# Performance work log

Hardware: AMD Instinct MI355X
Metric: run time of the kernel (lower is better)

The kernel has to match this reference:

```python
import jax, jax.numpy as jnp
import numpy as np

B, H, S, D = 2, 8, 4096, 64

def setup_inputs() -> dict:
    key = jax.random.key(0)
    kq, kk, kv = jax.random.split(key, 3)
    queries = jax.random.normal(kq, (B, H, S, D), dtype=jnp.float32)
    keys = jax.random.normal(kk, (B, H, S, D), dtype=jnp.float32)
    values = jax.random.normal(kv, (B, H, S, D), dtype=jnp.float32)
    adj = jnp.zeros((1,), dtype=jnp.int32)  # unused by the module, kept for signature fidelity
    return {"queries": queries, "keys": keys, "values": values, "adj": adj}

def reference(queries, keys, values, adj):
    # scores: [B,H,S,S]; note the original divides by a hard-coded 16, not sqrt(d)
    scores = jnp.einsum('bhqd,bhkd->bhqk', queries, keys) / 16.0
    attn = jax.nn.softmax(scores, axis=-1)
    # dropout p=0.0 -> identity in eval/deterministic mode
    h = jnp.einsum('bhqk,bhkd->bhqd', attn, values)  # [B,H,S,D]
    # original uses .view (a reshape, NOT a transpose) to (S, B, H, D)
    return jnp.reshape(h, (S, B, H, D))
```

## Files before the change

kernel.cpp:

```cpp
#include <hip/hip_runtime.h>
#include <hip/hip_bf16.h>
#include <math.h>

#define S_LEN 4096
#define D_DIM 64
#define NBH   16
#define HKT   32
#define QPRE  0.09016844f

typedef __attribute__((ext_vector_type(8))) short bf16x8;
typedef __attribute__((ext_vector_type(4))) float f32x4;
typedef __attribute__((ext_vector_type(16))) float f32x16;
typedef __attribute__((ext_vector_type(8))) __fp16 f16x8;
typedef __attribute__((ext_vector_type(2))) __fp16 f16x2;
typedef __attribute__((ext_vector_type(2))) unsigned int u32x2;

__device__ __forceinline__ unsigned int pkbf(float lo, float hi) {
  unsigned int ua = __float_as_uint(lo) + 0x8000u;
  unsigned int ub = __float_as_uint(hi) + 0x8000u;
  return __builtin_amdgcn_perm(ub, ua, 0x07060302u);
}
__device__ __forceinline__ unsigned int pkhf(float lo, float hi) {
  f16x2 h = __builtin_amdgcn_cvt_pkrtz(lo, hi);
  return *(unsigned int*)&h;
}
__device__ __forceinline__ void dma16(const unsigned short* g, unsigned short* l) {
  __builtin_amdgcn_global_load_lds(
      (const __attribute__((address_space(1))) unsigned int*)g,
      (__attribute__((address_space(3))) unsigned int*)l, 16, 0, 0);
}

__global__ __launch_bounds__(256) void prep(const float* __restrict__ K,
                                            const float* __restrict__ V,
                                            unsigned short* __restrict__ Kbf,
                                            unsigned short* __restrict__ Vt) {
  const int tid = threadIdx.x;
  __shared__ unsigned short tile[64][72];
  if (blockIdx.x < 256) {
    const int bh = blockIdx.x >> 4, ch = blockIdx.x & 15;
    const size_t base = ((size_t)bh * S_LEN + ch * 256) * D_DIM;
#pragma unroll
    for (int p = 0; p < 8; ++p) {
      int i = tid + p * 256;
      int row = i >> 3, c = (i & 7) * 8;
      float4 a = *(const float4*)&K[base + row * D_DIM + c];
      float4 b = *(const float4*)&K[base + row * D_DIM + c + 4];
      uint4 w;
      w.x = pkbf(a.x, a.y); w.y = pkbf(a.z, a.w);
      w.z = pkbf(b.x, b.y); w.w = pkbf(b.z, b.w);
      *(uint4*)&Kbf[base + row * D_DIM + c] = w;
    }
    return;
  }
  const int blk = blockIdx.x - 256;
  const int bh = blk >> 6, kt = blk & 63;
  const float* src = V + ((size_t)bh * S_LEN + kt * 64) * D_DIM;
#pragma unroll
  for (int p = 0; p < 4; ++p) {
    int i = tid + p * 256;
    int row = i >> 4, c = (i & 15) * 4;
    float4 f = *(const float4*)&src[row * D_DIM + c];
    int cs = c ^ (((row >> 4) & 3) << 4);
    unsigned long long w = (unsigned long long)pkhf(f.x, f.y) |
                           ((unsigned long long)pkhf(f.z, f.w) << 32);
    *(unsigned long long*)&tile[row][cs] = w;
  }
  __syncthreads();
  const int kc = tid & 7;
#pragma unroll
  for (int p = 0; p < 2; ++p) {
    int d = p * 32 + (tid >> 3);
    int col = d ^ (((kc >> 1) & 3) << 4);
    union { unsigned short u[8]; uint4 v; } t;
#pragma unroll
    for (int i = 0; i < 8; ++i) t.u[i] = tile[kc * 8 + i][col];
    *(uint4*)&Vt[((size_t)bh * D_DIM + d) * S_LEN + kt * 64 + kc * 8] = t.v;
  }
}

__global__ __launch_bounds__(256, 4) void fattn(const float* __restrict__ Q,
                                                const unsigned short* __restrict__ Kbf,
                                                const unsigned short* __restrict__ Vt,
                                                unsigned short* __restrict__ Oh,
                                                float* __restrict__ Lw) {
  const int bh   = blockIdx.x & 15;
  const int qb   = (blockIdx.x >> 4) & 31;
  const int half = blockIdx.x >> 9;
  const int tid  = threadIdx.x;
  const int wave = tid >> 6;
  const int lane = tid & 63;
  const int l31  = lane & 31;
  const int hi   = lane >> 5;
  const int T0   = half * HKT;

  __shared__ unsigned short Ksh[2][64][64];
  __shared__ unsigned short Vsh[2][64][64];

  bf16x8 qf2[4];
  {
    const int qg = qb * 128 + wave * 32 + l31;
    const float* qp = Q + ((size_t)bh * S_LEN + qg) * D_DIM + hi * 8;
#pragma unroll
    for (int dm = 0; dm < 4; ++dm) {
      float4 a = *(const float4*)&qp[dm * 16];
      float4 b = *(const float4*)&qp[dm * 16 + 4];
      union { unsigned int u[4]; bf16x8 v; } f;
      f.u[0] = pkbf(a.x * QPRE, a.y * QPRE);
      f.u[1] = pkbf(a.z * QPRE, a.w * QPRE);
      f.u[2] = pkbf(b.x * QPRE, b.y * QPRE);
      f.u[3] = pkbf(b.z * QPRE, b.w * QPRE);
      qf2[dm] = f.v;
    }
  }

  f32x16 ov[2] = {{}, {}};
  float Lt = 0.f;

  const unsigned short* Kb = Kbf + (size_t)bh * S_LEN * D_DIM;
  const unsigned short* Vb = Vt + (size_t)bh * D_DIM * S_LEN;

  const int r_lo = wave * 8 + (lane >> 3);
  const int csrc = ((lane & 7) ^ (lane >> 3)) * 8;

#define DMAK(T, B) do { const int t_ = (T); \
  dma16(&Kb[(size_t)(t_ * 64 + r_lo) * 64 + csrc],      &Ksh[B][wave * 8][0]); \
  dma16(&Kb[(size_t)(t_ * 64 + r_lo + 32) * 64 + csrc], &Ksh[B][wave * 8 + 32][0]); } while (0)
#define DMAV(T, B) do { const int t_ = (T); \
  dma16(&Vb[(size_t)r_lo * S_LEN + t_ * 64 + csrc],        &Vsh[B][wave * 8][0]); \
  dma16(&Vb[(size_t)(r_lo + 32) * S_LEN + t_ * 64 + csrc], &Vsh[B][wave * 8 + 32][0]); } while (0)

#define SCORES(KB, PD) do { \
  const char* kbase_ = (const char*)&Ksh[KB][0][0]; \
  _Pragma("unroll") \
  for (int kt2 = 0; kt2 < 2; ++kt2) { \
    const int krow_ = kt2 * 32 + l31; \
    f32x16 acc2 = {}; \
    _Pragma("unroll") \
    for (int dm = 0; dm < 4; ++dm) { \
      bf16x8 kf = *(const bf16x8*)(kbase_ + krow_ * 128 + (((dm * 2 + hi) ^ (krow_ & 7)) * 16)); \
      acc2 = __builtin_amdgcn_mfma_f32_32x32x16_bf16(kf, qf2[dm], acc2, 0, 0, 0); \
    } \
    float pp[16]; \
    _Pragma("unroll") \
    for (int j = 0; j < 16; ++j) pp[j] = __builtin_amdgcn_exp2f(acc2[j]); \
    Lt += (((pp[0] + pp[1]) + (pp[2] + pp[3])) + ((pp[4] + pp[5]) + (pp[6] + pp[7]))) \
        + (((pp[8] + pp[9]) + (pp[10] + pp[11])) + ((pp[12] + pp[13]) + (pp[14] + pp[15]))); \
    unsigned int w00 = pkhf(pp[0], pp[1]),   w01 = pkhf(pp[2], pp[3]); \
    unsigned int w10 = pkhf(pp[4], pp[5]),   w11 = pkhf(pp[6], pp[7]); \
    unsigned int w20 = pkhf(pp[8], pp[9]),   w21 = pkhf(pp[10], pp[11]); \
    unsigned int w30 = pkhf(pp[12], pp[13]), w31 = pkhf(pp[14], pp[15]); \
    u32x2 s0 = __builtin_amdgcn_permlane32_swap(w00, w10, false, false); \
    u32x2 s1 = __builtin_amdgcn_permlane32_swap(w01, w11, false, false); \
    u32x2 s2 = __builtin_amdgcn_permlane32_swap(w20, w30, false, false); \
    u32x2 s3 = __builtin_amdgcn_permlane32_swap(w21, w31, false, false); \
    PD[kt2 * 2 + 0][0] = s0.x; PD[kt2 * 2 + 0][1] = s1.x; \
    PD[kt2 * 2 + 0][2] = s0.y; PD[kt2 * 2 + 0][3] = s1.y; \
    PD[kt2 * 2 + 1][0] = s2.x; PD[kt2 * 2 + 1][1] = s3.x; \
    PD[kt2 * 2 + 1][2] = s2.y; PD[kt2 * 2 + 1][3] = s3.y; \
  } } while (0)

#define PVSTEP(VB, PU) do { \
  const char* vbase_ = (const char*)&Vsh[VB][0][0]; \
  _Pragma("unroll") \
  for (int dt2 = 0; dt2 < 2; ++dt2) { \
    const int drow_ = dt2 * 32 + l31; \
    _Pragma("unroll") \
    for (int s4 = 0; s4 < 4; ++s4) { \
      f16x8 va = *(const f16x8*)(vbase_ + drow_ * 128 + (((s4 * 2 + hi) ^ (drow_ & 7)) * 16)); \
      union { unsigned int u[4]; f16x8 v; } pb; \
      pb.u[0] = PU[s4][0]; pb.u[1] = PU[s4][1]; \
      pb.u[2] = PU[s4][2]; pb.u[3] = PU[s4][3]; \
      ov[dt2] = __builtin_amdgcn_mfma_f32_32x32x16_f16(va, pb.v, ov[dt2], 0, 0, 0); \
    } \
  } } while (0)

  unsigned int pA[4][4];

  DMAK(T0, 0); DMAV(T0, 0);
  __syncthreads();

  for (int b = 0; b < HKT - 2; b += 2) {
    DMAK(T0 + b + 1, 1); DMAV(T0 + b + 1, 1);
    SCORES(0, pA);
    PVSTEP(0, pA);
    __syncthreads();
    DMAK(T0 + b + 2, 0); DMAV(T0 + b + 2, 0);
    SCORES(1, pA);
    PVSTEP(1, pA);
    __syncthreads();
  }
  DMAK(T0 + HKT - 1, 1); DMAV(T0 + HKT - 1, 1);
  SCORES(0, pA);
  PVSTEP(0, pA);
  __syncthreads();
  SCORES(1, pA);
  PVSTEP(1, pA);

  Lt += __shfl_xor(Lt, 32);
  const size_t grow = (size_t)bh * S_LEN + qb * 128 + wave * 32 + l31;
  if (lane < 32) Lw[grow * 2 + half] = Lt;
#pragma unroll
  for (int dt2 = 0; dt2 < 2; ++dt2)
#pragma unroll
    for (int m = 0; m < 4; ++m) {
      uint2 w;
      w.x = pkhf(ov[dt2][4 * m + 0], ov[dt2][4 * m + 1]);
      w.y = pkhf(ov[dt2][4 * m + 2], ov[dt2][4 * m + 3]);
      *(uint2*)&Oh[grow * 128 + half * 64 + dt2 * 32 + m * 8 + hi * 4] = w;
    }
#undef DMAK
#undef DMAV
#undef SCORES
#undef PVSTEP
}

__global__ __launch_bounds__(256) void reduce(unsigned short* Oh, const float* __restrict__ Lw) {
  const int tid = threadIdx.x;
  const size_t r = (size_t)blockIdx.x * 32 + (tid >> 3);
  const int d0 = (tid & 7) * 8;
  union { uint4 v; __fp16 h[8]; } a, b;
  a.v = *(const uint4*)&Oh[r * 128 + d0];
  b.v = *(const uint4*)&Oh[r * 128 + 64 + d0];
  const float linv = 1.0f / (Lw[r * 2] + Lw[r * 2 + 1]);
  float o[8];
#pragma unroll
  for (int j = 0; j < 8; ++j) o[j] = ((float)a.h[j] + (float)b.h[j]) * linv;
  __syncthreads();
  float* Of = (float*)Oh;
  float4 w0 = {o[0], o[1], o[2], o[3]};
  float4 w1 = {o[4], o[5], o[6], o[7]};
  *(float4*)&Of[r * 64 + d0]     = w0;
  *(float4*)&Of[r * 64 + d0 + 4] = w1;
}

extern "C" void kernel_launch(void* const* d_in, const int* in_sizes, int n_in,
                              void* d_out, int out_size, void* d_ws, size_t ws_size,
                              hipStream_t stream) {
  const float* Q = (const float*)d_in[0];
  const float* K = (const float*)d_in[1];
  const float* V = (const float*)d_in[2];
  unsigned short* Kbf = (unsigned short*)d_ws;
  unsigned short* Vt  = Kbf + (size_t)NBH * S_LEN * D_DIM;
  float* Lw = (float*)(Vt + (size_t)NBH * S_LEN * D_DIM);
  unsigned short* Oh = (unsigned short*)d_out;

  prep<<<1280, 256, 0, stream>>>(K, V, Kbf, Vt);
  fattn<<<NBH * 32 * 2, 256, 0, stream>>>(Q, Kbf, Vt, Oh, Lw);
  reduce<<<(NBH * S_LEN) / 32, 256, 0, stream>>>(Oh, Lw);
}
```

Baseline: 178.1 us.

## Process two query sub-tiles per wave to reuse K/V fragments

Each wave now handles 64 query rows as two 32-row sub-tiles, loading each K and V fragment from shared memory once and feeding it to two MFMA chains. The grid shrinks to half as many blocks and the launch bound drops to 2 blocks per CU to allow the larger register footprint. This cuts LDS read traffic and staging per unit of compute, but reduces occupancy and the latency hiding it provides, and raises register pressure.

Result: slower. 201.4 us (+13.1%).

```diff
diff --git a/kernel.cpp b/kernel.cpp
--- a/kernel.cpp
+++ b/kernel.cpp
@@ -78,14 +78,14 @@
   }
 }
 
-__global__ __launch_bounds__(256, 4) void fattn(const float* __restrict__ Q,
+__global__ __launch_bounds__(256, 2) void fattn(const float* __restrict__ Q,
                                                 const unsigned short* __restrict__ Kbf,
                                                 const unsigned short* __restrict__ Vt,
                                                 unsigned short* __restrict__ Oh,
                                                 float* __restrict__ Lw) {
   const int bh   = blockIdx.x & 15;
-  const int qb   = (blockIdx.x >> 4) & 31;
-  const int half = blockIdx.x >> 9;
+  const int qb   = (blockIdx.x >> 4) & 15;
+  const int half = blockIdx.x >> 8;
   const int tid  = threadIdx.x;
   const int wave = tid >> 6;
   const int lane = tid & 63;
@@ -96,9 +96,10 @@
   __shared__ unsigned short Ksh[2][64][64];
   __shared__ unsigned short Vsh[2][64][64];
 
-  bf16x8 qf2[4];
-  {
-    const int qg = qb * 128 + wave * 32 + l31;
+  bf16x8 qf2[2][4];
+#pragma unroll
+  for (int qs = 0; qs < 2; ++qs) {
+    const int qg = qb * 256 + wave * 64 + qs * 32 + l31;
     const float* qp = Q + ((size_t)bh * S_LEN + qg) * D_DIM + hi * 8;
 #pragma unroll
     for (int dm = 0; dm < 4; ++dm) {
@@ -109,12 +110,12 @@
       f.u[1] = pkbf(a.z * QPRE, a.w * QPRE);
       f.u[2] = pkbf(b.x * QPRE, b.y * QPRE);
       f.u[3] = pkbf(b.z * QPRE, b.w * QPRE);
-      qf2[dm] = f.v;
+      qf2[qs][dm] = f.v;
     }
   }
 
-  f32x16 ov[2] = {{}, {}};
-  float Lt = 0.f;
+  f32x16 ov[2][2] = {{{}, {}}, {{}, {}}};
+  float Lq[2] = {0.f, 0.f};
 
   const unsigned short* Kb = Kbf + (size_t)bh * S_LEN * D_DIM;
   const unsigned short* Vb = Vt + (size_t)bh * D_DIM * S_LEN;
@@ -134,29 +135,34 @@
   _Pragma("unroll") \
   for (int kt2 = 0; kt2 < 2; ++kt2) { \
     const int krow_ = kt2 * 32 + l31; \
-    f32x16 acc2 = {}; \
+    bf16x8 kf_[4]; \
     _Pragma("unroll") \
-    for (int dm = 0; dm < 4; ++dm) { \
-      bf16x8 kf = *(const bf16x8*)(kbase_ + krow_ * 128 + (((dm * 2 + hi) ^ (krow_ & 7)) * 16)); \
-      acc2 = __builtin_amdgcn_mfma_f32_32x32x16_bf16(kf, qf2[dm], acc2, 0, 0, 0); \
+    for (int dm = 0; dm < 4; ++dm) \
+      kf_[dm] = *(const bf16x8*)(kbase_ + krow_ * 128 + (((dm * 2 + hi) ^ (krow_ & 7)) * 16)); \
+    _Pragma("unroll") \
+    for (int qs = 0; qs < 2; ++qs) { \
+      f32x16 acc2 = {}; \
+      _Pragma("unroll") \
+      for (int dm = 0; dm < 4; ++dm) \
+        acc2 = __builtin_amdgcn_mfma_f32_32x32x16_bf16(kf_[dm], qf2[qs][dm], acc2, 0, 0, 0); \
+      float pp[16]; \
+      _Pragma("unroll") \
+      for (int j = 0; j < 16; ++j) pp[j] = __builtin_amdgcn_exp2f(acc2[j]); \
+      Lq[qs] += (((pp[0] + pp[1]) + (pp[2] + pp[3])) + ((pp[4] + pp[5]) + (pp[6] + pp[7]))) \
+              + (((pp[8] + pp[9]) + (pp[10] + pp[11])) + ((pp[12] + pp[13]) + (pp[14] + pp[15]))); \
+      unsigned int w00 = pkhf(pp[0], pp[1]),   w01 = pkhf(pp[2], pp[3]); \
+      unsigned int w10 = pkhf(pp[4], pp[5]),   w11 = pkhf(pp[6], pp[7]); \
+      unsigned int w20 = pkhf(pp[8], pp[9]),   w21 = pkhf(pp[10], pp[11]); \
+      unsigned int w30 = pkhf(pp[12], pp[13]), w31 = pkhf(pp[14], pp[15]); \
+      u32x2 s0 = __builtin_amdgcn_permlane32_swap(w00, w10, false, false); \
+      u32x2 s1 = __builtin_amdgcn_permlane32_swap(w01, w11, false, false); \
+      u32x2 s2 = __builtin_amdgcn_permlane32_swap(w20, w30, false, false); \
+      u32x2 s3 = __builtin_amdgcn_permlane32_swap(w21, w31, false, false); \
+      PD[qs][kt2 * 2 + 0][0] = s0.x; PD[qs][kt2 * 2 + 0][1] = s1.x; \
+      PD[qs][kt2 * 2 + 0][2] = s0.y; PD[qs][kt2 * 2 + 0][3] = s1.y; \
+      PD[qs][kt2 * 2 + 1][0] = s2.x; PD[qs][kt2 * 2 + 1][1] = s3.x; \
+      PD[qs][kt2 * 2 + 1][2] = s2.y; PD[qs][kt2 * 2 + 1][3] = s3.y; \
     } \
-    float pp[16]; \
-    _Pragma("unroll") \
-    for (int j = 0; j < 16; ++j) pp[j] = __builtin_amdgcn_exp2f(acc2[j]); \
-    Lt += (((pp[0] + pp[1]) + (pp[2] + pp[3])) + ((pp[4] + pp[5]) + (pp[6] + pp[7]))) \
-        + (((pp[8] + pp[9]) + (pp[10] + pp[11])) + ((pp[12] + pp[13]) + (pp[14] + pp[15]))); \
-    unsigned int w00 = pkhf(pp[0], pp[1]),   w01 = pkhf(pp[2], pp[3]); \
-    unsigned int w10 = pkhf(pp[4], pp[5]),   w11 = pkhf(pp[6], pp[7]); \
-    unsigned int w20 = pkhf(pp[8], pp[9]),   w21 = pkhf(pp[10], pp[11]); \
-    unsigned int w30 = pkhf(pp[12], pp[13]), w31 = pkhf(pp[14], pp[15]); \
-    u32x2 s0 = __builtin_amdgcn_permlane32_swap(w00, w10, false, false); \
-    u32x2 s1 = __builtin_amdgcn_permlane32_swap(w01, w11, false, false); \
-    u32x2 s2 = __builtin_amdgcn_permlane32_swap(w20, w30, false, false); \
-    u32x2 s3 = __builtin_amdgcn_permlane32_swap(w21, w31, false, false); \
-    PD[kt2 * 2 + 0][0] = s0.x; PD[kt2 * 2 + 0][1] = s1.x; \
-    PD[kt2 * 2 + 0][2] = s0.y; PD[kt2 * 2 + 0][3] = s1.y; \
-    PD[kt2 * 2 + 1][0] = s2.x; PD[kt2 * 2 + 1][1] = s3.x; \
-    PD[kt2 * 2 + 1][2] = s2.y; PD[kt2 * 2 + 1][3] = s3.y; \
   } } while (0)
 
 #define PVSTEP(VB, PU) do { \
@@ -167,14 +173,17 @@
     _Pragma("unroll") \
     for (int s4 = 0; s4 < 4; ++s4) { \
       f16x8 va = *(const f16x8*)(vbase_ + drow_ * 128 + (((s4 * 2 + hi) ^ (drow_ & 7)) * 16)); \
-      union { unsigned int u[4]; f16x8 v; } pb; \
-      pb.u[0] = PU[s4][0]; pb.u[1] = PU[s4][1]; \
-      pb.u[2] = PU[s4][2]; pb.u[3] = PU[s4][3]; \
-      ov[dt2] = __builtin_amdgcn_mfma_f32_32x32x16_f16(va, pb.v, ov[dt2], 0, 0, 0); \
+      union { unsigned int u[4]; f16x8 v; } pb0, pb1; \
+      pb0.u[0] = PU[0][s4][0]; pb0.u[1] = PU[0][s4][1]; \
+      pb0.u[2] = PU[0][s4][2]; pb0.u[3] = PU[0][s4][3]; \
+      pb1.u[0] = PU[1][s4][0]; pb1.u[1] = PU[1][s4][1]; \
+      pb1.u[2] = PU[1][s4][2]; pb1.u[3] = PU[1][s4][3]; \
+      ov[0][dt2] = __builtin_amdgcn_mfma_f32_32x32x16_f16(va, pb0.v, ov[0][dt2], 0, 0, 0); \
+      ov[1][dt2] = __builtin_amdgcn_mfma_f32_32x32x16_f16(va, pb1.v, ov[1][dt2], 0, 0, 0); \
     } \
   } } while (0)
 
-  unsigned int pA[4][4];
+  unsigned int pA[2][4][4];
 
   DMAK(T0, 0); DMAV(T0, 0);
   __syncthreads();
@@ -196,18 +205,22 @@
   SCORES(1, pA);
   PVSTEP(1, pA);
 
-  Lt += __shfl_xor(Lt, 32);
-  const size_t grow = (size_t)bh * S_LEN + qb * 128 + wave * 32 + l31;
-  if (lane < 32) Lw[grow * 2 + half] = Lt;
-#pragma unroll
-  for (int dt2 = 0; dt2 < 2; ++dt2)
-#pragma unroll
-    for (int m = 0; m < 4; ++m) {
-      uint2 w;
-      w.x = pkhf(ov[dt2][4 * m + 0], ov[dt2][4 * m + 1]);
-      w.y = pkhf(ov[dt2][4 * m + 2], ov[dt2][4 * m + 3]);
-      *(uint2*)&Oh[grow * 128 + half * 64 + dt2 * 32 + m * 8 + hi * 4] = w;
-    }
+#pragma unroll
+  for (int qs = 0; qs < 2; ++qs) {
+    float Lts = Lq[qs];
+    Lts += __shfl_xor(Lts, 32);
+    const size_t grow = (size_t)bh * S_LEN + qb * 256 + wave * 64 + qs * 32 + l31;
+    if (lane < 32) Lw[grow * 2 + half] = Lts;
+#pragma unroll
+    for (int dt2 = 0; dt2 < 2; ++dt2)
+#pragma unroll
+      for (int m = 0; m < 4; ++m) {
+        uint2 w;
+        w.x = pkhf(ov[qs][dt2][4 * m + 0], ov[qs][dt2][4 * m + 1]);
+        w.y = pkhf(ov[qs][dt2][4 * m + 2], ov[qs][dt2][4 * m + 3]);
+        *(uint2*)&Oh[grow * 128 + half * 64 + dt2 * 32 + m * 8 + hi * 4] = w;
+      }
+  }
 #undef DMAK
 #undef DMAV
 #undef SCORES
@@ -245,6 +258,6 @@
   unsigned short* Oh = (unsigned short*)d_out;
 
   prep<<<1280, 256, 0, stream>>>(K, V, Kbf, Vt);
-  fattn<<<NBH * 32 * 2, 256, 0, stream>>>(Q, Kbf, Vt, Oh, Lw);
+  fattn<<<NBH * 16 * 2, 256, 0, stream>>>(Q, Kbf, Vt, Oh, Lw);
   reduce<<<(NBH * S_LEN) / 32, 256, 0, stream>>>(Oh, Lw);
 }
```

## Fuse split-K reduction into attention kernel via last-block atomic counter

Applied to the files above, without the earlier changes.

Drops the separate reduce kernel. Each attention block now bumps a per-(head, query-block) atomic counter after writing its half, and the second block to finish merges both fp16 partial outputs with the softmax denominators and writes the fp32 result in place. The counters are zeroed in the prep kernel, and the Lw layout changes to half-major. This removes one kernel launch and its serial pass over memory, at the cost of a threadfence, an atomic, and a tail of work on the last-finishing blocks.

Result: slower. 370.3 us (+107.9%).

```diff
diff --git a/kernel.cpp b/kernel.cpp
--- a/kernel.cpp
+++ b/kernel.cpp
@@ -6,6 +6,7 @@
 #define D_DIM 64
 #define NBH   16
 #define HKT   32
+#define NROW  (NBH * S_LEN)
 #define QPRE  0.09016844f
 
 typedef __attribute__((ext_vector_type(8))) short bf16x8;
@@ -33,10 +34,12 @@
 __global__ __launch_bounds__(256) void prep(const float* __restrict__ K,
                                             const float* __restrict__ V,
                                             unsigned short* __restrict__ Kbf,
-                                            unsigned short* __restrict__ Vt) {
+                                            unsigned short* __restrict__ Vt,
+                                            int* __restrict__ flags) {
   const int tid = threadIdx.x;
   __shared__ unsigned short tile[64][72];
   if (blockIdx.x < 256) {
+    if (blockIdx.x == 0) { flags[tid] = 0; flags[tid + 256] = 0; }
     const int bh = blockIdx.x >> 4, ch = blockIdx.x & 15;
     const size_t base = ((size_t)bh * S_LEN + ch * 256) * D_DIM;
 #pragma unroll
@@ -82,7 +85,8 @@
                                                 const unsigned short* __restrict__ Kbf,
                                                 const unsigned short* __restrict__ Vt,
                                                 unsigned short* __restrict__ Oh,
-                                                float* __restrict__ Lw) {
+                                                float* __restrict__ Lw,
+                                                int* __restrict__ flags) {
   const int bh   = blockIdx.x & 15;
   const int qb   = (blockIdx.x >> 4) & 31;
   const int half = blockIdx.x >> 9;
@@ -95,6 +99,7 @@
 
   __shared__ unsigned short Ksh[2][64][64];
   __shared__ unsigned short Vsh[2][64][64];
+  __shared__ int last;
 
   bf16x8 qf2[4];
   {
@@ -198,7 +203,7 @@
 
   Lt += __shfl_xor(Lt, 32);
   const size_t grow = (size_t)bh * S_LEN + qb * 128 + wave * 32 + l31;
-  if (lane < 32) Lw[grow * 2 + half] = Lt;
+  if (lane < 32) Lw[(size_t)half * NROW + grow] = Lt;
 #pragma unroll
   for (int dt2 = 0; dt2 < 2; ++dt2)
 #pragma unroll
@@ -208,29 +213,38 @@
       w.y = pkhf(ov[dt2][4 * m + 2], ov[dt2][4 * m + 3]);
       *(uint2*)&Oh[grow * 128 + half * 64 + dt2 * 32 + m * 8 + hi * 4] = w;
     }
+
+  __threadfence();
+  __syncthreads();
+  if (tid == 0) last = atomicAdd(&flags[(bh << 5) | qb], 1);
+  __syncthreads();
+  if (last == 1) {
+    __threadfence();
+    const size_t base = (size_t)bh * S_LEN + qb * 128;
+    float* Of = (float*)Oh;
+#pragma unroll
+    for (int p = 0; p < 2; ++p) {
+      const size_t row = base + p * 64 + (tid >> 2);
+      const int d0 = (tid & 3) * 16;
+      union { uint4 v[2]; __fp16 h[16]; } A, B;
+      A.v[0] = *(const uint4*)&Oh[row * 128 + d0];
+      A.v[1] = *(const uint4*)&Oh[row * 128 + d0 + 8];
+      B.v[0] = *(const uint4*)&Oh[row * 128 + 64 + d0];
+      B.v[1] = *(const uint4*)&Oh[row * 128 + 64 + d0 + 8];
+      const float linv = 1.0f / (Lw[row] + Lw[(size_t)NROW + row]);
+      float o[16];
+#pragma unroll
+      for (int j = 0; j < 16; ++j) o[j] = ((float)A.h[j] + (float)B.h[j]) * linv;
+      *(float4*)&Of[row * 64 + d0 + 0]  = *(float4*)&o[0];
+      *(float4*)&Of[row * 64 + d0 + 4]  = *(float4*)&o[4];
+      *(float4*)&Of[row * 64 + d0 + 8]  = *(float4*)&o[8];
+      *(float4*)&Of[row * 64 + d0 + 12] = *(float4*)&o[12];
+    }
+  }
 #undef DMAK
 #undef DMAV
 #undef SCORES
 #undef PVSTEP
-}
-
-__global__ __launch_bounds__(256) void reduce(unsigned short* Oh, const float* __restrict__ Lw) {
-  const int tid = threadIdx.x;
-  const size_t r = (size_t)blockIdx.x * 32 + (tid >> 3);
-  const int d0 = (tid & 7) * 8;
-  union { uint4 v; __fp16 h[8]; } a, b;
-  a.v = *(const uint4*)&Oh[r * 128 + d0];
-  b.v = *(const uint4*)&Oh[r * 128 + 64 + d0];
-  const float linv = 1.0f / (Lw[r * 2] + Lw[r * 2 + 1]);
-  float o[8];
-#pragma unroll
-  for (int j = 0; j < 8; ++j) o[j] = ((float)a.h[j] + (float)b.h[j]) * linv;
-  __syncthreads();
-  float* Of = (float*)Oh;
-  float4 w0 = {o[0], o[1], o[2], o[3]};
-  float4 w1 = {o[4], o[5], o[6], o[7]};
-  *(float4*)&Of[r * 64 + d0]     = w0;
-  *(float4*)&Of[r * 64 + d0 + 4] = w1;
 }
 
 extern "C" void kernel_launch(void* const* d_in, const int* in_sizes, int n_in,
@@ -242,9 +256,9 @@
   unsigned short* Kbf = (unsigned short*)d_ws;
   unsigned short* Vt  = Kbf + (size_t)NBH * S_LEN * D_DIM;
   float* Lw = (float*)(Vt + (size_t)NBH * S_LEN * D_DIM);
+  int* flags = (int*)(Lw + 2 * (size_t)NROW);
   unsigned short* Oh = (unsigned short*)d_out;
 
-  prep<<<1280, 256, 0, stream>>>(K, V, Kbf, Vt);
-  fattn<<<NBH * 32 * 2, 256, 0, stream>>>(Q, Kbf, Vt, Oh, Lw);
-  reduce<<<(NBH * S_LEN) / 32, 256, 0, stream>>>(Oh, Lw);
-}
+  prep<<<1280, 256, 0, stream>>>(K, V, Kbf, Vt, flags);
+  fattn<<<NBH * 32 * 2, 256, 0, stream>>>(Q, Kbf, Vt, Oh, Lw, flags);
+}
```

## Drop split-KV and reduce kernel; normalize output directly in attention kernel

Applied to the files above, without the earlier changes.

Removes the two-way split over the key sequence, so each block processes all 64 KV tiles and writes normalized fp32 output directly. This eliminates the separate reduce kernel launch and the fp16 partial-output and row-sum round trip through memory. In exchange the grid is halved to 512 blocks, which lowers parallelism and occupancy on a large GPU and doubles per-block serial work.

Result: faster. 169.7 us (-4.7%).

```diff
diff --git a/kernel.cpp b/kernel.cpp
--- a/kernel.cpp
+++ b/kernel.cpp
@@ -5,7 +5,7 @@
 #define S_LEN 4096
 #define D_DIM 64
 #define NBH   16
-#define HKT   32
+#define NKT   64
 #define QPRE  0.09016844f
 
 typedef __attribute__((ext_vector_type(8))) short bf16x8;
@@ -81,17 +81,14 @@
 __global__ __launch_bounds__(256, 4) void fattn(const float* __restrict__ Q,
                                                 const unsigned short* __restrict__ Kbf,
                                                 const unsigned short* __restrict__ Vt,
-                                                unsigned short* __restrict__ Oh,
-                                                float* __restrict__ Lw) {
+                                                float* __restrict__ Of) {
   const int bh   = blockIdx.x & 15;
-  const int qb   = (blockIdx.x >> 4) & 31;
-  const int half = blockIdx.x >> 9;
+  const int qb   = blockIdx.x >> 4;
   const int tid  = threadIdx.x;
   const int wave = tid >> 6;
   const int lane = tid & 63;
   const int l31  = lane & 31;
   const int hi   = lane >> 5;
-  const int T0   = half * HKT;
 
   __shared__ unsigned short Ksh[2][64][64];
   __shared__ unsigned short Vsh[2][64][64];
@@ -176,20 +173,20 @@
 
   unsigned int pA[4][4];
 
-  DMAK(T0, 0); DMAV(T0, 0);
+  DMAK(0, 0); DMAV(0, 0);
   __syncthreads();
 
-  for (int b = 0; b < HKT - 2; b += 2) {
-    DMAK(T0 + b + 1, 1); DMAV(T0 + b + 1, 1);
+  for (int b = 0; b < NKT - 2; b += 2) {
+    DMAK(b + 1, 1); DMAV(b + 1, 1);
     SCORES(0, pA);
     PVSTEP(0, pA);
     __syncthreads();
-    DMAK(T0 + b + 2, 0); DMAV(T0 + b + 2, 0);
+    DMAK(b + 2, 0); DMAV(b + 2, 0);
     SCORES(1, pA);
     PVSTEP(1, pA);
     __syncthreads();
   }
-  DMAK(T0 + HKT - 1, 1); DMAV(T0 + HKT - 1, 1);
+  DMAK(NKT - 1, 1); DMAV(NKT - 1, 1);
   SCORES(0, pA);
   PVSTEP(0, pA);
   __syncthreads();
@@ -197,40 +194,20 @@
   PVSTEP(1, pA);
 
   Lt += __shfl_xor(Lt, 32);
+  const float linv = 1.0f / Lt;
   const size_t grow = (size_t)bh * S_LEN + qb * 128 + wave * 32 + l31;
-  if (lane < 32) Lw[grow * 2 + half] = Lt;
 #pragma unroll
   for (int dt2 = 0; dt2 < 2; ++dt2)
 #pragma unroll
     for (int m = 0; m < 4; ++m) {
-      uint2 w;
-      w.x = pkhf(ov[dt2][4 * m + 0], ov[dt2][4 * m + 1]);
-      w.y = pkhf(ov[dt2][4 * m + 2], ov[dt2][4 * m + 3]);
-      *(uint2*)&Oh[grow * 128 + half * 64 + dt2 * 32 + m * 8 + hi * 4] = w;
+      float4 w = {ov[dt2][4 * m + 0] * linv, ov[dt2][4 * m + 1] * linv,
+                  ov[dt2][4 * m + 2] * linv, ov[dt2][4 * m + 3] * linv};
+      *(float4*)&Of[grow * 64 + dt2 * 32 + m * 8 + hi * 4] = w;
     }
 #undef DMAK
 #undef DMAV
 #undef SCORES
 #undef PVSTEP
-}
-
-__global__ __launch_bounds__(256) void reduce(unsigned short* Oh, const float* __restrict__ Lw) {
-  const int tid = threadIdx.x;
-  const size_t r = (size_t)blockIdx.x * 32 + (tid >> 3);
-  const int d0 = (tid & 7) * 8;
-  union { uint4 v; __fp16 h[8]; } a, b;
-  a.v = *(const uint4*)&Oh[r * 128 + d0];
-  b.v = *(const uint4*)&Oh[r * 128 + 64 + d0];
-  const float linv = 1.0f / (Lw[r * 2] + Lw[r * 2 + 1]);
-  float o[8];
-#pragma unroll
-  for (int j = 0; j < 8; ++j) o[j] = ((float)a.h[j] + (float)b.h[j]) * linv;
-  __syncthreads();
-  float* Of = (float*)Oh;
-  float4 w0 = {o[0], o[1], o[2], o[3]};
-  float4 w1 = {o[4], o[5], o[6], o[7]};
-  *(float4*)&Of[r * 64 + d0]     = w0;
-  *(float4*)&Of[r * 64 + d0 + 4] = w1;
 }
 
 extern "C" void kernel_launch(void* const* d_in, const int* in_sizes, int n_in,
@@ -241,10 +218,8 @@
   const float* V = (const float*)d_in[2];
   unsigned short* Kbf = (unsigned short*)d_ws;
   unsigned short* Vt  = Kbf + (size_t)NBH * S_LEN * D_DIM;
-  float* Lw = (float*)(Vt + (size_t)NBH * S_LEN * D_DIM);
-  unsigned short* Oh = (unsigned short*)d_out;
+  float* Of = (float*)d_out;
 
   prep<<<1280, 256, 0, stream>>>(K, V, Kbf, Vt);
-  fattn<<<NBH * 32 * 2, 256, 0, stream>>>(Q, Kbf, Vt, Oh, Lw);
-  reduce<<<(NBH * S_LEN) / 32, 256, 0, stream>>>(Oh, Lw);
-}
+  fattn<<<NBH * 32, 256, 0, stream>>>(Q, Kbf, Vt, Of);
+}
```
